# Kernel tuning notes

Hardware: AMD Instinct MI355X
Metric: run time of the kernel (lower is better)

## Reference

```python
import jax, jax.numpy as jnp
import numpy as np

NUM_GRID = 16
GRID_SIZE = 8  # 128 / NUM_GRID
H = W = 128
BN_EPS = 1e-5


def conv2d(x, w, b, pad):
    y = jax.lax.conv_general_dilated(
        x, w, window_strides=(1, 1), padding=[(pad, pad), (pad, pad)],
        dimension_numbers=('NCHW', 'OIHW', 'NCHW'))
    return y + b[None, :, None, None]


def bn(x, g, be, m, v):
    # inference-mode BatchNorm2d with running stats
    inv = g / jnp.sqrt(v + BN_EPS)
    return x * inv[None, :, None, None] + (be - m * inv)[None, :, None, None]


def setup_inputs() -> dict:
    key = jax.random.key(0)
    ks = jax.random.split(key, 6)
    def wconv(k, o, i, s):
        return jax.random.normal(k, (o, i, s, s), jnp.float32) * (1.0 / np.sqrt(i * s * s))
    return {
        'x': jax.random.uniform(ks[0], (64, 1, 128, 128), jnp.float32),
        'w1': wconv(ks[1], 64, 1, 3), 'b1': jnp.zeros((64,), jnp.float32),
        'g1': jnp.ones((64,), jnp.float32), 'be1': jnp.zeros((64,), jnp.float32),
        'm1': jnp.zeros((64,), jnp.float32), 'v1': jnp.ones((64,), jnp.float32),
        'w2': wconv(ks[2], 32, 64, 3), 'b2': jnp.zeros((32,), jnp.float32),
        'g2': jnp.ones((32,), jnp.float32), 'be2': jnp.zeros((32,), jnp.float32),
        'm2': jnp.zeros((32,), jnp.float32), 'v2': jnp.ones((32,), jnp.float32),
        'w3': wconv(ks[3], 32, 32, 3), 'b3': jnp.zeros((32,), jnp.float32),
        'g3': jnp.ones((32,), jnp.float32), 'be3': jnp.zeros((32,), jnp.float32),
        'm3': jnp.zeros((32,), jnp.float32), 'v3': jnp.ones((32,), jnp.float32),
        'w4': wconv(ks[4], 1, 32, 3), 'b4': jnp.zeros((1,), jnp.float32),
    }


def reference(x, w1, b1, g1, be1, m1, v1, w2, b2, g2, be2, m2, v2,
              w3, b3, g3, be3, m3, v3, w4, b4):
    # EncoderAttentionNodes.forward, phase='train', expressed with static shapes:
    # instead of torch.nonzero gather of valid grids, compute per-grid node
    # coordinates for ALL 16x16 grids and return a validity mask. The math per
    # valid grid is identical (the rect mask is a rectangular 8x8 block, so
    # masking + normalization reduce to block-local weighted sums).
    B = x.shape[0]
    h = jax.nn.relu(bn(conv2d(x, w1, b1, 4), g1, be1, m1, v1))   # [B,64,134,134]
    h = jax.nn.relu(bn(conv2d(h, w2, b2, 0), g2, be2, m2, v2))   # [B,32,132,132]
    h = jax.nn.relu(bn(conv2d(h, w3, b3, 0), g3, be3, m3, v3))   # [B,32,130,130]
    heat_raw = conv2d(h, w4, b4, 0)                              # [B,1,128,128]
    heat = jax.nn.sigmoid(heat_raw)[:, 0]                        # [B,128,128]

    # block view: [B, yi, ya, xj, xc] with yi,xj grid indices and ya,xc in-block
    hb = heat.reshape(B, NUM_GRID, GRID_SIZE, NUM_GRID, GRID_SIZE)
    grid = hb.max(axis=(2, 4)).reshape(B, NUM_GRID * NUM_GRID)   # maxpool 8x8 s8
    sorted_grid = jnp.sort(grid, axis=1)[:, ::-1]                # descending
    thresh = jnp.maximum(sorted_grid[:, 16], 0.9)[:, None]       # train phase
    valid = grid > thresh                                        # [B,256]

    xref = jnp.linspace(0.0, 1.0, W).reshape(NUM_GRID, GRID_SIZE)
    yref = jnp.linspace(0.0, 1.0, H).reshape(NUM_GRID, GRID_SIZE)
    s = hb.sum(axis=(2, 4))                                      # [B,16,16] block mass
    sx = jnp.einsum('biajc,jc->bij', hb, xref)
    sy = jnp.einsum('biajc,ia->bij', hb, yref)
    nodes = jnp.stack([sx / s, sy / s], axis=-1)                 # [B,16,16,2]
    nodes = nodes.reshape(B, NUM_GRID * NUM_GRID, 2)
    nodes = jnp.where(valid[:, :, None], nodes, 0.0)             # zero padded slots
    nodes_per_image = valid.sum(axis=1).astype(jnp.int32)        # == torch.bincount
    return nodes, heat_raw, valid, nodes_per_image
```

## Files before the change

kernel.cpp:

```cpp
#include <hip/hip_runtime.h>
#include <math.h>

#define BN_EPS 1e-5f

typedef _Float16 half8 __attribute__((ext_vector_type(8)));
typedef float f32x4 __attribute__((ext_vector_type(4)));

__global__ __launch_bounds__(256) void prep_kernel(
    const float* __restrict__ w1, const float* __restrict__ b1,
    const float* __restrict__ g1, const float* __restrict__ be1,
    const float* __restrict__ m1, const float* __restrict__ v1,
    const float* __restrict__ w2, const float* __restrict__ b2,
    const float* __restrict__ g2, const float* __restrict__ be2,
    const float* __restrict__ m2, const float* __restrict__ v2,
    const float* __restrict__ w3, const float* __restrict__ b3,
    const float* __restrict__ g3, const float* __restrict__ be3,
    const float* __restrict__ m3, const float* __restrict__ v3,
    char* __restrict__ ws)
{
    float* w1e = (float*)ws;
    float* b1e = (float*)(ws + 2304);
    float* b2e = (float*)(ws + 2560);
    float* b3e = (float*)(ws + 2688);
    _Float16* wT2e = (_Float16*)(ws + 2816);
    _Float16* wT3e = (_Float16*)(ws + 39680);

    for (int t = threadIdx.x; t < 576; t += 256) {
        int oc = t / 9;
        float inv = g1[oc] * rsqrtf(v1[oc] + BN_EPS);
        w1e[t] = w1[t] * inv;
    }
    for (int t = threadIdx.x; t < 64; t += 256) {
        float inv = g1[t] * rsqrtf(v1[t] + BN_EPS);
        b1e[t] = b1[t] * inv + be1[t] - m1[t] * inv;
    }
    for (int t = threadIdx.x; t < 32; t += 256) {
        float inv2 = g2[t] * rsqrtf(v2[t] + BN_EPS);
        b2e[t] = b2[t] * inv2 + be2[t] - m2[t] * inv2;
        float inv3 = g3[t] * rsqrtf(v3[t] + BN_EPS);
        b3e[t] = b3[t] * inv3 + be3[t] - m3[t] * inv3;
    }
    for (int t = threadIdx.x; t < 18432; t += 256) {
        int r = t / 2048; int rem = t - r * 2048;
        int oc = rem >> 6; int ic = rem & 63;
        float inv = g2[oc] * rsqrtf(v2[oc] + BN_EPS);
        wT2e[t] = (_Float16)(w2[(oc * 64 + ic) * 9 + r] * inv);
    }
    for (int t = threadIdx.x; t < 9216; t += 256) {
        int r = t / 1024; int rem = t - r * 1024;
        int oc = rem >> 5; int ic = rem & 31;
        float inv = g3[oc] * rsqrtf(v3[oc] + BN_EPS);
        wT3e[t] = (_Float16)(w3[(oc * 32 + ic) * 9 + r] * inv);
    }
}

__global__ __launch_bounds__(256, 4) void f12_kernel(
    const float* __restrict__ x, const char* __restrict__ wsw,
    _Float16* __restrict__ h2)
{
    const float* w1e = (const float*)wsw;
    const float* b1e = (const float*)(wsw + 2304);
    const float* b2e = (const float*)(wsw + 2560);
    const _Float16* wT2e = (const _Float16*)(wsw + 2816);

    constexpr int PSTR = 36;
    __shared__ float sX[20 * 20];
    __shared__ _Float16 sH1[324 * PSTR];

    const int t = threadIdx.x, lane = t & 63, w = t >> 6;
    const int tl = lane & 15, g = lane >> 4;
    const int img = blockIdx.z;
    const int x0 = blockIdx.x * 16, y0 = blockIdx.y * 16;

    const float* xb = x + (size_t)img * 16384;
    for (int idx = t; idx < 400; idx += 256) {
        int r = idx / 20, c = idx - r * 20;
        int iy = y0 - 4 + r, ix = x0 - 4 + c;
        sX[idx] = (iy >= 0 && iy < 128 && ix >= 0 && ix < 128)
                      ? xb[iy * 128 + ix] : 0.f;
    }
    __syncthreads();

    f32x4 acc[4][2];
#pragma unroll
    for (int pf = 0; pf < 4; pf++)
#pragma unroll
        for (int of = 0; of < 2; of++) acc[pf][of] = (f32x4){0.f, 0.f, 0.f, 0.f};

#pragma unroll
    for (int h = 0; h < 2; h++) {
        {
            const int ocg = __builtin_amdgcn_readfirstlane(t >> 6);
            const int pxslot = t & 63;
            float wreg[8][9];
            float bb[8];
#pragma unroll
            for (int j = 0; j < 8; j++) {
                int oc = h * 32 + ocg * 8 + j;
                bb[j] = b1e[oc];
#pragma unroll
                for (int k = 0; k < 9; k++) wreg[j][k] = w1e[oc * 9 + k];
            }
#pragma unroll
            for (int round = 0; round < 6; round++) {
                int px = pxslot + round * 64;
                if (px < 324) {
                    int py = px / 18, pxx = px - py * 18;
                    float a[9];
#pragma unroll
                    for (int ky = 0; ky < 3; ky++)
#pragma unroll
                        for (int kx = 0; kx < 3; kx++)
                            a[ky * 3 + kx] = sX[(py + ky) * 20 + pxx + kx];
                    half8 hv;
#pragma unroll
                    for (int j = 0; j < 8; j++) {
                        float acc1 = bb[j];
#pragma unroll
                        for (int k = 0; k < 9; k++)
                            acc1 = fmaf(a[k], wreg[j][k], acc1);
                        hv[j] = (_Float16)fmaxf(acc1, 0.f);
                    }
                    *(half8*)(&sH1[px * PSTR + ocg * 8]) = hv;
                }
            }
        }
        __syncthreads();

        {
            half8 wf[9][2];
#pragma unroll
            for (int r = 0; r < 9; r++)
#pragma unroll
                for (int of = 0; of < 2; of++)
                    wf[r][of] = *(const half8*)(
                        wT2e + (r * 32 + of * 16 + tl) * 64 + h * 32 + g * 8);
#pragma unroll
            for (int r = 0; r < 9; r++) {
                const int ky = r / 3, kx = r - ky * 3;
#pragma unroll
                for (int pf = 0; pf < 4; pf++) {
                    const int yl = w * 4 + pf + ky;
                    half8 af = *(const half8*)(
                        &sH1[(yl * 18 + tl + kx) * PSTR + g * 8]);
                    acc[pf][0] = __builtin_amdgcn_mfma_f32_16x16x32_f16(
                        af, wf[r][0], acc[pf][0], 0, 0, 0);
                    acc[pf][1] = __builtin_amdgcn_mfma_f32_16x16x32_f16(
                        af, wf[r][1], acc[pf][1], 0, 0, 0);
                }
            }
        }
        if (h == 0) __syncthreads();
    }

    const float bb0 = b2e[tl], bb1 = b2e[16 + tl];
    _Float16* outb = h2 + (size_t)img * 132 * 132 * 32;
#pragma unroll
    for (int pf = 0; pf < 4; pf++) {
        int y = y0 + w * 4 + pf;
        if (y >= 132) continue;
#pragma unroll
        for (int i = 0; i < 4; i++) {
            int xc = x0 + 4 * g + i;
            if (xc >= 132) continue;
            _Float16* q = outb + ((size_t)y * 132 + xc) * 32 + tl;
            q[0]  = (_Float16)fmaxf(acc[pf][0][i] + bb0, 0.f);
            q[16] = (_Float16)fmaxf(acc[pf][1][i] + bb1, 0.f);
        }
    }
}

__global__ __launch_bounds__(256, 4) void conv3_kernel(
    const _Float16* __restrict__ in, const char* __restrict__ wsw,
    _Float16* __restrict__ out)
{
    const float* b3e = (const float*)(wsw + 2688);
    const _Float16* wT3e = (const _Float16*)(wsw + 39680);

    constexpr int HIN = 132, WIN = 132, HOUT = 130, WOUT = 130;
    constexpr int PSTR = 40;
    __shared__ _Float16 sIn[324 * PSTR];

    const int t = threadIdx.x, lane = t & 63, w = t >> 6;
    const int tl = lane & 15, g = lane >> 4;
    const int img = 63 - blockIdx.z;
    const int x0 = blockIdx.x * 16, y0 = blockIdx.y * 16;

    const _Float16* inb = in + (size_t)img * HIN * WIN * 32;

    for (int kk = 0; kk < 6; kk++) {
        int idx = t + kk * 256;
        if (idx < 1296) {
            int px = idx >> 2, sg = idx & 3;
            int py = px / 18, pxx = px - py * 18;
            int iy = y0 + py, ix = x0 + pxx;
            half8 v = (half8){0, 0, 0, 0, 0, 0, 0, 0};
            if (iy < HIN && ix < WIN)
                v = *(const half8*)(inb + ((size_t)iy * WIN + ix) * 32 + sg * 8);
            *(half8*)(&sIn[px * PSTR + sg * 8]) = v;
        }
    }

    half8 wf[9][2];
#pragma unroll
    for (int r = 0; r < 9; r++)
#pragma unroll
        for (int of = 0; of < 2; of++)
            wf[r][of] = *(const half8*)(
                wT3e + (r * 32 + of * 16 + tl) * 32 + g * 8);

    f32x4 acc[4][2];
#pragma unroll
    for (int pf = 0; pf < 4; pf++)
#pragma unroll
        for (int of = 0; of < 2; of++) acc[pf][of] = (f32x4){0.f, 0.f, 0.f, 0.f};

    __syncthreads();

#pragma unroll
    for (int r = 0; r < 9; r++) {
        const int ky = r / 3, kx = r - ky * 3;
#pragma unroll
        for (int pf = 0; pf < 4; pf++) {
            const int yl = w * 4 + pf + ky;
            half8 af = *(const half8*)(&sIn[(yl * 18 + tl + kx) * PSTR + g * 8]);
            acc[pf][0] = __builtin_amdgcn_mfma_f32_16x16x32_f16(
                af, wf[r][0], acc[pf][0], 0, 0, 0);
            acc[pf][1] = __builtin_amdgcn_mfma_f32_16x16x32_f16(
                af, wf[r][1], acc[pf][1], 0, 0, 0);
        }
    }

    const float bb0 = b3e[tl], bb1 = b3e[16 + tl];
    _Float16* outb = out + (size_t)img * HOUT * WOUT * 32;
#pragma unroll
    for (int pf = 0; pf < 4; pf++) {
        int y = y0 + w * 4 + pf;
        if (y >= HOUT) continue;
#pragma unroll
        for (int i = 0; i < 4; i++) {
            int xc = x0 + 4 * g + i;
            if (xc >= WOUT) continue;
            _Float16* q = outb + ((size_t)y * WOUT + xc) * 32 + tl;
            q[0]  = (_Float16)fmaxf(acc[pf][0][i] + bb0, 0.f);
            q[16] = (_Float16)fmaxf(acc[pf][1][i] + bb1, 0.f);
        }
    }
}

__global__ __launch_bounds__(256) void conv4_kernel(
    const _Float16* __restrict__ h3, const float* __restrict__ w4,
    const float* __restrict__ b4, float* __restrict__ heat)
{
    int b = blockIdx.z;
    int sp = blockIdx.x * 256 + threadIdx.x;
    int y = sp >> 7, x = sp & 127;

    __shared__ float sw[288];
    for (int i = threadIdx.x; i < 288; i += 256) sw[i] = w4[i];
    __syncthreads();

    const _Float16* hb = h3 + (size_t)b * 130 * 130 * 32;
    float acc = b4[0];
#pragma unroll
    for (int r = 0; r < 9; r++) {
        const int ky = r / 3, kx = r - ky * 3;
        const _Float16* p = hb + ((size_t)(y + ky) * 130 + (x + kx)) * 32;
        half8 v0 = *(const half8*)(p);
        half8 v1 = *(const half8*)(p + 8);
        half8 v2 = *(const half8*)(p + 16);
        half8 v3 = *(const half8*)(p + 24);
#pragma unroll
        for (int j = 0; j < 8; j++) {
            acc = fmaf((float)v0[j], sw[(j) * 9 + r], acc);
            acc = fmaf((float)v1[j], sw[(8 + j) * 9 + r], acc);
            acc = fmaf((float)v2[j], sw[(16 + j) * 9 + r], acc);
            acc = fmaf((float)v3[j], sw[(24 + j) * 9 + r], acc);
        }
    }
    heat[(size_t)b * 16384 + sp] = acc;
}

__global__ __launch_bounds__(256) void nodes_kernel(
    const float* __restrict__ heat_raw, float* __restrict__ nodes,
    float* __restrict__ valid, float* __restrict__ counts)
{
    int b = blockIdx.x;
    int gsl = threadIdx.x;
    int yi = gsl >> 4, xj = gsl & 15;
    const float* hb = heat_raw + (size_t)b * 16384;

    float mx = -1e30f, s = 0.f, sx = 0.f, sy = 0.f;
#pragma unroll
    for (int a = 0; a < 8; a++) {
        int row = yi * 8 + a;
        float yr = (float)row * (1.0f / 127.0f);
#pragma unroll
        for (int c = 0; c < 8; c++) {
            int col = xj * 8 + c;
            float hv = hb[row * 128 + col];
            float hs = 1.0f / (1.0f + expf(-hv));
            mx = fmaxf(mx, hs);
            s += hs;
            sx += hs * ((float)col * (1.0f / 127.0f));
            sy += hs * yr;
        }
    }

    __shared__ float gv[256];
    gv[gsl] = mx;
    __syncthreads();

    int cgt = 0, ceq = 0;
    for (int j = 0; j < 256; j++) {
        float vj = gv[j];
        cgt += (vj > mx) ? 1 : 0;
        ceq += (vj == mx) ? 1 : 0;
    }
    __shared__ float kth;
    if (cgt <= 16 && 16 < cgt + ceq) kth = mx;
    __syncthreads();

    float thresh = fmaxf(kth, 0.9f);
    bool val = mx > thresh;
    nodes[((size_t)b * 256 + gsl) * 2 + 0] = val ? sx / s : 0.f;
    nodes[((size_t)b * 256 + gsl) * 2 + 1] = val ? sy / s : 0.f;
    valid[(size_t)b * 256 + gsl] = val ? 1.f : 0.f;

    unsigned long long ball = __ballot(val);
    __shared__ int wc[4];
    if ((gsl & 63) == 0) wc[gsl >> 6] = __popcll(ball);
    __syncthreads();
    if (gsl == 0) counts[b] = (float)(wc[0] + wc[1] + wc[2] + wc[3]);
}

extern "C" void kernel_launch(void* const* d_in, const int* in_sizes, int n_in,
                              void* d_out, int out_size, void* d_ws, size_t ws_size,
                              hipStream_t stream)
{
    const float* x   = (const float*)d_in[0];
    const float* w1  = (const float*)d_in[1];
    const float* b1  = (const float*)d_in[2];
    const float* g1  = (const float*)d_in[3];
    const float* be1 = (const float*)d_in[4];
    const float* m1  = (const float*)d_in[5];
    const float* v1  = (const float*)d_in[6];
    const float* w2  = (const float*)d_in[7];
    const float* b2  = (const float*)d_in[8];
    const float* g2  = (const float*)d_in[9];
    const float* be2 = (const float*)d_in[10];
    const float* m2  = (const float*)d_in[11];
    const float* v2  = (const float*)d_in[12];
    const float* w3  = (const float*)d_in[13];
    const float* b3  = (const float*)d_in[14];
    const float* g3  = (const float*)d_in[15];
    const float* be3 = (const float*)d_in[16];
    const float* m3  = (const float*)d_in[17];
    const float* v3  = (const float*)d_in[18];
    const float* w4  = (const float*)d_in[19];
    const float* b4  = (const float*)d_in[20];

    float* out = (float*)d_out;
    float* out_nodes = out;
    float* out_heat  = out + 32768;
    float* out_valid = out + 32768 + 1048576;
    float* out_count = out + 32768 + 1048576 + 16384;

    char* ws = (char*)d_ws;
    const size_t WREGION = 65536;
    _Float16* h2 = (_Float16*)(ws + WREGION);
    _Float16* h3 = h2 + (size_t)64 * 17424 * 32;

    prep_kernel<<<1, 256, 0, stream>>>(w1, b1, g1, be1, m1, v1,
                                       w2, b2, g2, be2, m2, v2,
                                       w3, b3, g3, be3, m3, v3, ws);

    dim3 gd(9, 9, 64);
    f12_kernel<<<gd, 256, 0, stream>>>(x, ws, h2);
    conv3_kernel<<<gd, 256, 0, stream>>>(h2, ws, h3);

    dim3 gd4(64, 1, 64);
    conv4_kernel<<<gd4, 256, 0, stream>>>(h3, w4, b4, out_heat);

    nodes_kernel<<<64, 256, 0, stream>>>(out_heat, out_nodes, out_valid, out_count);
}
```

Baseline: 268.6 us.

## Fuse per-cell heat statistics into conv4 and stream weights per tap

conv4 now uses 16x16 spatial tiles and computes sigmoid, max, sum and weighted coordinate sums for each 8x8 cell with wave shuffles. It writes the per-cell stats to workspace, so the nodes kernel only reads those stats and does the threshold selection. This removes the serial 64-element loop per thread and the extra read of the heat map in the nodes kernel. Separately, conv2/conv3 load MFMA weight fragments per tap instead of preloading all 18, and occupancy hints drop from 4 to 3, which trades load latency for lower register pressure.

```diff
diff --git a/kernel.cpp b/kernel.cpp
--- a/kernel.cpp
+++ b/kernel.cpp
@@ -54,7 +54,7 @@
     }
 }
 
-__global__ __launch_bounds__(256, 4) void f12_kernel(
+__global__ __launch_bounds__(256, 3) void f12_kernel(
     const float* __restrict__ x, const char* __restrict__ wsw,
     _Float16* __restrict__ h2)
 {
@@ -127,27 +127,22 @@
         }
         __syncthreads();
 
-        {
-            half8 wf[9][2];
-#pragma unroll
-            for (int r = 0; r < 9; r++)
-#pragma unroll
-                for (int of = 0; of < 2; of++)
-                    wf[r][of] = *(const half8*)(
-                        wT2e + (r * 32 + of * 16 + tl) * 64 + h * 32 + g * 8);
-#pragma unroll
-            for (int r = 0; r < 9; r++) {
-                const int ky = r / 3, kx = r - ky * 3;
-#pragma unroll
-                for (int pf = 0; pf < 4; pf++) {
-                    const int yl = w * 4 + pf + ky;
-                    half8 af = *(const half8*)(
-                        &sH1[(yl * 18 + tl + kx) * PSTR + g * 8]);
-                    acc[pf][0] = __builtin_amdgcn_mfma_f32_16x16x32_f16(
-                        af, wf[r][0], acc[pf][0], 0, 0, 0);
-                    acc[pf][1] = __builtin_amdgcn_mfma_f32_16x16x32_f16(
-                        af, wf[r][1], acc[pf][1], 0, 0, 0);
-                }
+#pragma unroll
+        for (int r = 0; r < 9; r++) {
+            const int ky = r / 3, kx = r - ky * 3;
+            half8 wf0 = *(const half8*)(
+                wT2e + (r * 32 + tl) * 64 + h * 32 + g * 8);
+            half8 wf1 = *(const half8*)(
+                wT2e + (r * 32 + 16 + tl) * 64 + h * 32 + g * 8);
+#pragma unroll
+            for (int pf = 0; pf < 4; pf++) {
+                const int yl = w * 4 + pf + ky;
+                half8 af = *(const half8*)(
+                    &sH1[(yl * 18 + tl + kx) * PSTR + g * 8]);
+                acc[pf][0] = __builtin_amdgcn_mfma_f32_16x16x32_f16(
+                    af, wf0, acc[pf][0], 0, 0, 0);
+                acc[pf][1] = __builtin_amdgcn_mfma_f32_16x16x32_f16(
+                    af, wf1, acc[pf][1], 0, 0, 0);
             }
         }
         if (h == 0) __syncthreads();
@@ -170,7 +165,7 @@
     }
 }
 
-__global__ __launch_bounds__(256, 4) void conv3_kernel(
+__global__ __launch_bounds__(256, 3) void conv3_kernel(
     const _Float16* __restrict__ in, const char* __restrict__ wsw,
     _Float16* __restrict__ out)
 {
@@ -201,14 +196,6 @@
         }
     }
 
-    half8 wf[9][2];
-#pragma unroll
-    for (int r = 0; r < 9; r++)
-#pragma unroll
-        for (int of = 0; of < 2; of++)
-            wf[r][of] = *(const half8*)(
-                wT3e + (r * 32 + of * 16 + tl) * 32 + g * 8);
-
     f32x4 acc[4][2];
 #pragma unroll
     for (int pf = 0; pf < 4; pf++)
@@ -220,14 +207,16 @@
 #pragma unroll
     for (int r = 0; r < 9; r++) {
         const int ky = r / 3, kx = r - ky * 3;
+        half8 wf0 = *(const half8*)(wT3e + (r * 32 + tl) * 32 + g * 8);
+        half8 wf1 = *(const half8*)(wT3e + (r * 32 + 16 + tl) * 32 + g * 8);
 #pragma unroll
         for (int pf = 0; pf < 4; pf++) {
             const int yl = w * 4 + pf + ky;
             half8 af = *(const half8*)(&sIn[(yl * 18 + tl + kx) * PSTR + g * 8]);
             acc[pf][0] = __builtin_amdgcn_mfma_f32_16x16x32_f16(
-                af, wf[r][0], acc[pf][0], 0, 0, 0);
+                af, wf0, acc[pf][0], 0, 0, 0);
             acc[pf][1] = __builtin_amdgcn_mfma_f32_16x16x32_f16(
-                af, wf[r][1], acc[pf][1], 0, 0, 0);
+                af, wf1, acc[pf][1], 0, 0, 0);
         }
     }
 
@@ -250,17 +239,21 @@
 
 __global__ __launch_bounds__(256) void conv4_kernel(
     const _Float16* __restrict__ h3, const float* __restrict__ w4,
-    const float* __restrict__ b4, float* __restrict__ heat)
-{
-    int b = blockIdx.z;
-    int sp = blockIdx.x * 256 + threadIdx.x;
-    int y = sp >> 7, x = sp & 127;
+    const float* __restrict__ b4, float* __restrict__ heat,
+    float* __restrict__ stats)
+{
+    const int img = blockIdx.z;
+    const int x0 = blockIdx.x * 16, y0 = blockIdx.y * 16;
+    const int t = threadIdx.x;
+    const int ty = t >> 4, tx = t & 15;
 
     __shared__ float sw[288];
-    for (int i = threadIdx.x; i < 288; i += 256) sw[i] = w4[i];
-    __syncthreads();
-
-    const _Float16* hb = h3 + (size_t)b * 130 * 130 * 32;
+    __shared__ float sS[256];
+    for (int i = t; i < 288; i += 256) sw[i] = w4[i];
+    __syncthreads();
+
+    const int y = y0 + ty, x = x0 + tx;
+    const _Float16* hb = h3 + (size_t)img * 130 * 130 * 32;
     float acc = b4[0];
 #pragma unroll
     for (int r = 0; r < 9; r++) {
@@ -278,34 +271,39 @@
             acc = fmaf((float)v3[j], sw[(24 + j) * 9 + r], acc);
         }
     }
-    heat[(size_t)b * 16384 + sp] = acc;
-}
-
-__global__ __launch_bounds__(256) void nodes_kernel(
-    const float* __restrict__ heat_raw, float* __restrict__ nodes,
+    heat[(size_t)img * 16384 + y * 128 + x] = acc;
+    sS[t] = 1.0f / (1.0f + expf(-acc));
+    __syncthreads();
+
+    const int w = t >> 6, l = t & 63;
+    const int cy = w >> 1, cx = w & 1;
+    const int ly = cy * 8 + (l >> 3), lx = cx * 8 + (l & 7);
+    float v = sS[ly * 16 + lx];
+    float mx = v, s = v;
+    float sx = v * ((float)(x0 + lx) * (1.0f / 127.0f));
+    float sy = v * ((float)(y0 + ly) * (1.0f / 127.0f));
+#pragma unroll
+    for (int off = 1; off < 64; off <<= 1) {
+        mx = fmaxf(mx, __shfl_xor(mx, off));
+        s += __shfl_xor(s, off);
+        sx += __shfl_xor(sx, off);
+        sy += __shfl_xor(sy, off);
+    }
+    if (l == 0) {
+        int cell = (blockIdx.y * 2 + cy) * 16 + blockIdx.x * 2 + cx;
+        float4* st = (float4*)(stats + ((size_t)img * 256 + cell) * 4);
+        *st = make_float4(mx, s, sx, sy);
+    }
+}
+
+__global__ __launch_bounds__(256) void nodes2_kernel(
+    const float* __restrict__ stats, float* __restrict__ nodes,
     float* __restrict__ valid, float* __restrict__ counts)
 {
     int b = blockIdx.x;
     int gsl = threadIdx.x;
-    int yi = gsl >> 4, xj = gsl & 15;
-    const float* hb = heat_raw + (size_t)b * 16384;
-
-    float mx = -1e30f, s = 0.f, sx = 0.f, sy = 0.f;
-#pragma unroll
-    for (int a = 0; a < 8; a++) {
-        int row = yi * 8 + a;
-        float yr = (float)row * (1.0f / 127.0f);
-#pragma unroll
-        for (int c = 0; c < 8; c++) {
-            int col = xj * 8 + c;
-            float hv = hb[row * 128 + col];
-            float hs = 1.0f / (1.0f + expf(-hv));
-            mx = fmaxf(mx, hs);
-            s += hs;
-            sx += hs * ((float)col * (1.0f / 127.0f));
-            sy += hs * yr;
-        }
-    }
+    float4 st = ((const float4*)stats)[b * 256 + gsl];
+    float mx = st.x, s = st.y, sx = st.z, sy = st.w;
 
     __shared__ float gv[256];
     gv[gsl] = mx;
@@ -368,7 +366,8 @@
 
     char* ws = (char*)d_ws;
     const size_t WREGION = 65536;
-    _Float16* h2 = (_Float16*)(ws + WREGION);
+    float* stats = (float*)(ws + WREGION);
+    _Float16* h2 = (_Float16*)(ws + WREGION + 262144);
     _Float16* h3 = h2 + (size_t)64 * 17424 * 32;
 
     prep_kernel<<<1, 256, 0, stream>>>(w1, b1, g1, be1, m1, v1,
@@ -379,8 +378,8 @@
     f12_kernel<<<gd, 256, 0, stream>>>(x, ws, h2);
     conv3_kernel<<<gd, 256, 0, stream>>>(h2, ws, h3);
 
-    dim3 gd4(64, 1, 64);
-    conv4_kernel<<<gd4, 256, 0, stream>>>(h3, w4, b4, out_heat);
-
-    nodes_kernel<<<64, 256, 0, stream>>>(out_heat, out_nodes, out_valid, out_count);
-}
+    dim3 gd4(8, 8, 64);
+    conv4_kernel<<<gd4, 256, 0, stream>>>(h3, w4, b4, out_heat, stats);
+
+    nodes2_kernel<<<64, 256, 0, stream>>>(stats, out_nodes, out_valid, out_count);
+}
```

Result: faster. 241.3 us (-10.1%).
